# Kernel optimization log

Measured on AMD Instinct MI355X. Metric: run time of the kernel, lower is better.

The kernel has to match this reference:

```python
import jax, jax.numpy as jnp
import numpy as np

IMG_SIZE = 512
NUM_FREQ_MASKS = 4


def _make_masks(n, num):
    # Mirrors DCTTransform._generate_freq_masks: for i in reversed(range(num-1)),
    # an anti-triangular (low-frequency) mask of size n//2**i padded to (n,n),
    # then an all-ones mask appended last.
    masks = []
    for i in reversed(range(num - 1)):
        m = n // (2 ** i)
        tri = np.triu(np.ones((m, m), dtype=np.float32))      # upper triangular
        rot = np.rot90(tri, k=1)                               # -> i+j <= m-1 region
        pad = np.zeros((n, n), dtype=np.float32)
        pad[:m, :m] = rot
        masks.append(pad)
    masks.append(np.ones((n, n), dtype=np.float32))
    return np.stack(masks)  # [num, n, n]


def _dct_matrix(n, dtype=jnp.float32):
    # Orthonormal DCT-II matrix: X = D @ x  ==  scipy.fftpack.dct(x, axis=0, norm='ortho')
    k = jnp.arange(n, dtype=dtype)[:, None]
    m = jnp.arange(n, dtype=dtype)[None, :]
    D = jnp.cos(jnp.pi * (2.0 * m + 1.0) * k / (2.0 * n)) * jnp.sqrt(2.0 / n)
    D = D.at[0].multiply(1.0 / jnp.sqrt(2.0))  # k=0 row scale -> sqrt(1/n)
    return D


def setup_inputs() -> dict:
    key = jax.random.key(0)
    x = jax.random.normal(key, (32, 3, IMG_SIZE, IMG_SIZE), dtype=jnp.float32)
    masks = jnp.asarray(_make_masks(IMG_SIZE, NUM_FREQ_MASKS))
    return {"x": x, "masks": masks}


def reference(x, masks):
    # x: [B, C, H, W] with H == W == img_size; masks: [4, H, W]
    n = x.shape[-1]
    D = _dct_matrix(n, x.dtype)
    # 2D orthonormal DCT-II over last two axes: D @ x @ D^T (separable, order-free)
    dct2 = jnp.einsum('ij,bcjk,lk->bcil', D, x, D)
    outs = []
    for i in range(masks.shape[0]):  # small fixed loop over 4 masks
        masked = dct2 * masks[i]
        # inverse 2D DCT (IDCT-II == DCT-III, orthonormal): D^T @ y @ D
        outs.append(jnp.einsum('ji,bcjk,kl->bcil', D, masked, D))
    LH, HL, HH, LL = outs  # idx 0->LH, 1->HL, 2->HH, 3(ones)->LL per original forward
    return (LL, LH, HL, HH)
```

## Files before the change

kernel.cpp:

```cpp
#include <hip/hip_runtime.h>
#include <hip/hip_bf16.h>
#include <stdint.h>

#define NIMG 96
#define N 512
#define IMG (N*N)
#define OUT_PLANE ((long long)NIMG * IMG)

typedef __attribute__((ext_vector_type(8))) _Float16 f16x8;
typedef __attribute__((ext_vector_type(4))) float f32x4;
typedef unsigned short u16;

__device__ inline u16 f2h(float v) {
    _Float16 h = (_Float16)v;
    return __builtin_bit_cast(u16, h);
}

__device__ inline void gload16(const void* g, void* l) {
    __builtin_amdgcn_global_load_lds(
        (const __attribute__((address_space(1))) void*)g,
        (__attribute__((address_space(3))) void*)l, 16, 0, 0);
}

__global__ void build_D(u16* __restrict__ Drm, u16* __restrict__ Dcm) {
    int idx = blockIdx.x * 256 + threadIdx.x;
    int k = idx >> 9, m = idx & 511;
    int r = ((2 * m + 1) * k) & 2047;
    float c = cospif((float)r * (1.0f / 1024.0f));
    float s = (k == 0) ? 0.04419417382415922f : 0.0625f;
    u16 h = f2h(c * s);
    Drm[k * 512 + m] = h;
    Dcm[m * 512 + k] = h;
}

__global__ __launch_bounds__(256) void conv_x(const float* __restrict__ x,
                                              u16* __restrict__ Xcm,
                                              float* __restrict__ outLL) {
    __shared__ float t[32][33];
    const long long base = (long long)blockIdx.z * IMG;
    const int r0 = blockIdx.y * 32, c0 = blockIdx.x * 32;
    const int tr = threadIdx.x >> 3;
    const int tc = (threadIdx.x & 7) * 4;
    float4 v = *(const float4*)&x[base + (long long)(r0 + tr) * N + c0 + tc];
    *(float4*)&outLL[base + (long long)(r0 + tr) * N + c0 + tc] = v;
    t[tr][tc + 0] = v.x; t[tr][tc + 1] = v.y;
    t[tr][tc + 2] = v.z; t[tr][tc + 3] = v.w;
    __syncthreads();
    ushort4 h;
    h.x = f2h(t[tc + 0][tr]); h.y = f2h(t[tc + 1][tr]);
    h.z = f2h(t[tc + 2][tr]); h.w = f2h(t[tc + 3][tr]);
    *(ushort4*)&Xcm[base + (long long)(c0 + tr) * N + r0 + tc] = h;
}

template<int EPI>
__global__ __launch_bounds__(256) void gemm16(
    const u16* __restrict__ A, long long sA, int lda,
    const u16* __restrict__ B, long long sB, int ldb,
    void* __restrict__ Cv, long long sC, int ldc,
    int K, int trilim, int kcap,
    u16* __restrict__ Y2, u16* __restrict__ Y3)
{
    __shared__ u16 As[2][128 * 32];
    __shared__ u16 Bs[2][128 * 32];

    const int bz = blockIdx.z;
    const int m0 = blockIdx.y * 128;
    const int n0 = blockIdx.x * 128;
    const int tid = threadIdx.x;
    const int wave = tid >> 6;
    const int lane = tid & 63;

    const u16* __restrict__ Ab = A + (long long)bz * sA;
    const u16* __restrict__ Bb = B + (long long)bz * sB;

    const int srow = lane >> 2;
    const int sc8  = (lane & 3) * 8;
    const int war  = wave * 32;

    const int fr  = lane & 15;
    const int kg8 = (lane >> 4) * 8;
    const int wr  = (wave >> 1) * 64;
    const int wc  = (wave & 1) * 64;

    int aoff[4], boff[4];
    #pragma unroll
    for (int i = 0; i < 4; ++i) {
        aoff[i] = (wr + i * 16 + fr) * 32 + kg8;
        boff[i] = (wc + i * 16 + fr) * 32 + kg8;
    }

    f32x4 acc[4][4];
    #pragma unroll
    for (int i = 0; i < 4; ++i)
        #pragma unroll
        for (int j = 0; j < 4; ++j)
            acc[i][j] = (f32x4){0.0f, 0.0f, 0.0f, 0.0f};

    const bool skip = (EPI == 3) && (m0 + n0 > trilim);
    const int Keff = (kcap - m0 < K) ? (kcap - m0) : K;

    if (!skip) {
        auto stage = [&](int buf, int k0) {
            #pragma unroll
            for (int i = 0; i < 2; ++i) {
                int r = war + i * 16;
                gload16(Ab + (long long)(m0 + r + srow) * lda + k0 + sc8, &As[buf][r * 32]);
                gload16(Bb + (long long)(n0 + r + srow) * ldb + k0 + sc8, &Bs[buf][r * 32]);
            }
        };
        auto compute = [&](int buf) {
            f16x8 af[4], bf[4];
            #pragma unroll
            for (int i = 0; i < 4; ++i) af[i] = *(const f16x8*)&As[buf][aoff[i]];
            #pragma unroll
            for (int j = 0; j < 4; ++j) bf[j] = *(const f16x8*)&Bs[buf][boff[j]];
            #pragma unroll
            for (int i = 0; i < 4; ++i)
                #pragma unroll
                for (int j = 0; j < 4; ++j)
                    acc[i][j] = __builtin_amdgcn_mfma_f32_16x16x32_f16(af[i], bf[j], acc[i][j], 0, 0, 0);
        };

        const int nb = Keff >> 5;
        stage(0, 0);
        __syncthreads();
        int cur = 0;
        for (int t = 0; t < nb - 1; ++t) {
            stage(cur ^ 1, (t + 1) * 32);
            compute(cur);
            __syncthreads();
            cur ^= 1;
        }
        compute(cur);
    }

    const int rb = (lane >> 4) * 4;
    if (EPI == 0) {
        float* Cb = (float*)Cv + (long long)bz * sC;
        #pragma unroll
        for (int i = 0; i < 4; ++i)
            #pragma unroll
            for (int j = 0; j < 4; ++j) {
                int r = m0 + wr + i * 16 + rb;
                int c = n0 + wc + j * 16 + fr;
                #pragma unroll
                for (int g = 0; g < 4; ++g)
                    Cb[(long long)(r + g) * ldc + c] = acc[i][j][g];
            }
    } else if (EPI == 1) {
        u16* Cb = (u16*)Cv + (long long)bz * sC;
        #pragma unroll
        for (int i = 0; i < 4; ++i)
            #pragma unroll
            for (int j = 0; j < 4; ++j) {
                int r = m0 + wr + i * 16 + rb;
                int c = n0 + wc + j * 16 + fr;
                #pragma unroll
                for (int g = 0; g < 4; ++g)
                    Cb[(long long)(r + g) * ldc + c] = f2h(acc[i][j][g]);
            }
    } else {
        u16* Cb = (u16*)Cv + (long long)bz * sC;
        u16* Y2b = (EPI == 3) ? Y2 + (long long)bz * (256 * 256) : nullptr;
        u16* Y3b = (EPI == 3) ? Y3 + (long long)bz * (128 * 128) : nullptr;
        #pragma unroll
        for (int i = 0; i < 4; ++i)
            #pragma unroll
            for (int j = 0; j < 4; ++j) {
                int r = m0 + wr + i * 16 + rb;
                int c = n0 + wc + j * 16 + fr;
                float v0 = ((r + 0) + c <= trilim) ? acc[i][j][0] : 0.0f;
                float v1 = ((r + 1) + c <= trilim) ? acc[i][j][1] : 0.0f;
                float v2 = ((r + 2) + c <= trilim) ? acc[i][j][2] : 0.0f;
                float v3 = ((r + 3) + c <= trilim) ? acc[i][j][3] : 0.0f;
                ushort4 h;
                h.x = f2h(v0); h.y = f2h(v1); h.z = f2h(v2); h.w = f2h(v3);
                *(ushort4*)&Cb[(long long)c * ldc + r] = h;
                if (EPI == 3) {
                    if (r < 256 && c < 256) {
                        ushort4 h2;
                        h2.x = ((r + 0) + c <= 255) ? h.x : (u16)0;
                        h2.y = ((r + 1) + c <= 255) ? h.y : (u16)0;
                        h2.z = ((r + 2) + c <= 255) ? h.z : (u16)0;
                        h2.w = ((r + 3) + c <= 255) ? h.w : (u16)0;
                        *(ushort4*)&Y2b[(long long)c * 256 + r] = h2;
                    }
                    if (r < 128 && c < 128) {
                        ushort4 h3;
                        h3.x = ((r + 0) + c <= 127) ? h.x : (u16)0;
                        h3.y = ((r + 1) + c <= 127) ? h.y : (u16)0;
                        h3.z = ((r + 2) + c <= 127) ? h.z : (u16)0;
                        h3.w = ((r + 3) + c <= 127) ? h.w : (u16)0;
                        *(ushort4*)&Y3b[(long long)c * 128 + r] = h3;
                    }
                }
            }
    }
}

extern "C" void kernel_launch(void* const* d_in, const int* in_sizes, int n_in,
                              void* d_out, int out_size, void* d_ws, size_t ws_size,
                              hipStream_t stream) {
    const float* x = (const float*)d_in[0];
    float* out = (float*)d_out;
    float* outLL = out + 0 * OUT_PLANE;
    float* outLH = out + 1 * OUT_PLANE;
    float* outHL = out + 2 * OUT_PLANE;
    float* outHH = out + 3 * OUT_PLANE;

    char* ws = (char*)d_ws;
    u16* Drm = (u16*)(ws);
    u16* Dcm = (u16*)(ws + 524288);
    u16* Xcm = (u16*)(ws + 1048576);
    u16* Ycm = Xcm;
    char* reg = ws + 51380224;
    u16* T1 = (u16*)reg;
    u16* U  = (u16*)reg;
    u16* U2 = (u16*)reg;
    u16* U3 = (u16*)reg;
    u16* Y2 = (u16*)outLH;
    u16* Y3 = (u16*)outLH + (long long)NIMG * 256 * 256;

    const long long S = IMG;
    const int BIG = 1 << 30;

    build_D<<<dim3(IMG / 256), 256, 0, stream>>>(Drm, Dcm);
    conv_x<<<dim3(16, 16, NIMG), 256, 0, stream>>>(x, Xcm, outLL);

    gemm16<1><<<dim3(4, 4, NIMG), 256, 0, stream>>>(
        Drm, 0, 512, Xcm, S, 512, T1, S, 512, 512, 0, BIG, nullptr, nullptr);
    gemm16<3><<<dim3(4, 4, NIMG), 256, 0, stream>>>(
        T1, S, 512, Drm, 0, 512, Ycm, S, 512, 512, 511, BIG, Y2, Y3);
    gemm16<2><<<dim3(4, 4, NIMG), 256, 0, stream>>>(
        Ycm, S, 512, Dcm, 0, 512, U, S, 512, 512, BIG, 512, nullptr, nullptr);
    gemm16<0><<<dim3(4, 4, NIMG), 256, 0, stream>>>(
        U, S, 512, Dcm, 0, 512, outHH, S, 512, 512, 0, BIG, nullptr, nullptr);

    gemm16<2><<<dim3(4, 2, NIMG), 256, 0, stream>>>(
        Y2, 256 * 256, 256, Dcm, 0, 512, U2, 512 * 256, 256, 256, BIG, 256, nullptr, nullptr);
    gemm16<0><<<dim3(4, 4, NIMG), 256, 0, stream>>>(
        U2, 512 * 256, 256, Dcm, 0, 512, outHL, S, 512, 256, 0, BIG, nullptr, nullptr);

    gemm16<2><<<dim3(4, 1, NIMG), 256, 0, stream>>>(
        Y3, 128 * 128, 128, Dcm, 0, 512, U3, 512 * 128, 128, 128, BIG, BIG, nullptr, nullptr);
    gemm16<0><<<dim3(4, 4, NIMG), 256, 0, stream>>>(
        U3, 512 * 128, 128, Dcm, 0, 512, outLH, S, 512, 128, 0, BIG, nullptr, nullptr);
}
```

Measured before the change: 366.4 us.

## Merge inverse-DCT GEMMs for the three masked bands into batched multi-problem launches

New measurement: 355.2 us. 3.1% less time.

```diff
diff --git a/kernel.cpp b/kernel.cpp
--- a/kernel.cpp
+++ b/kernel.cpp
@@ -11,12 +11,12 @@
 typedef __attribute__((ext_vector_type(4))) float f32x4;
 typedef unsigned short u16;
 
-__device__ inline u16 f2h(float v) {
+__device__ __forceinline__ u16 f2h(float v) {
     _Float16 h = (_Float16)v;
     return __builtin_bit_cast(u16, h);
 }
 
-__device__ inline void gload16(const void* g, void* l) {
+__device__ __forceinline__ void gload16(const void* g, void* l) {
     __builtin_amdgcn_global_load_lds(
         (const __attribute__((address_space(1))) void*)g,
         (__attribute__((address_space(3))) void*)l, 16, 0, 0);
@@ -52,89 +52,88 @@
     *(ushort4*)&Xcm[base + (long long)(c0 + tr) * N + r0 + tc] = h;
 }
 
+#define GEMM_DECLS                                                         \
+    const int tid = threadIdx.x;                                           \
+    const int wave = tid >> 6;                                             \
+    const int lane = tid & 63;                                             \
+    const int srow = lane >> 2;                                            \
+    const int sc8  = (lane & 3) * 8;                                       \
+    const int war  = wave * 32;                                            \
+    const int fr   = lane & 15;                                            \
+    const int kg8  = (lane >> 4) * 8;                                      \
+    const int wr   = (wave >> 1) * 64;                                     \
+    const int wc   = (wave & 1) * 64;                                      \
+    const int rb   = (lane >> 4) * 4;                                      \
+    int aoff[4], boff[4];                                                  \
+    _Pragma("unroll")                                                      \
+    for (int i = 0; i < 4; ++i) {                                          \
+        aoff[i] = (wr + i * 16 + fr) * 32 + kg8;                           \
+        boff[i] = (wc + i * 16 + fr) * 32 + kg8;                           \
+    }                                                                      \
+    f32x4 acc[4][4];                                                       \
+    _Pragma("unroll")                                                      \
+    for (int i = 0; i < 4; ++i)                                            \
+        _Pragma("unroll")                                                  \
+        for (int j = 0; j < 4; ++j)                                        \
+            acc[i][j] = (f32x4){0.0f, 0.0f, 0.0f, 0.0f};
+
+#define GEMM_LOOP(Ab, lda, Bb, ldb, Keff)                                  \
+    {                                                                      \
+        auto stage = [&](int buf, int k0) {                                \
+            _Pragma("unroll")                                              \
+            for (int i = 0; i < 2; ++i) {                                  \
+                int r = war + i * 16;                                      \
+                gload16((Ab) + (long long)(m0 + r + srow) * (lda) + k0 + sc8, &As[buf][r * 32]); \
+                gload16((Bb) + (long long)(n0 + r + srow) * (ldb) + k0 + sc8, &Bs[buf][r * 32]); \
+            }                                                              \
+        };                                                                 \
+        auto compute = [&](int buf) {                                      \
+            f16x8 af[4], bf[4];                                            \
+            _Pragma("unroll")                                              \
+            for (int i = 0; i < 4; ++i) af[i] = *(const f16x8*)&As[buf][aoff[i]]; \
+            _Pragma("unroll")                                              \
+            for (int j = 0; j < 4; ++j) bf[j] = *(const f16x8*)&Bs[buf][boff[j]]; \
+            _Pragma("unroll")                                              \
+            for (int i = 0; i < 4; ++i)                                    \
+                _Pragma("unroll")                                          \
+                for (int j = 0; j < 4; ++j)                                \
+                    acc[i][j] = __builtin_amdgcn_mfma_f32_16x16x32_f16(af[i], bf[j], acc[i][j], 0, 0, 0); \
+        };                                                                 \
+        const int nb = (Keff) >> 5;                                        \
+        stage(0, 0);                                                       \
+        __syncthreads();                                                   \
+        int cur = 0;                                                       \
+        for (int t = 0; t < nb - 1; ++t) {                                 \
+            stage(cur ^ 1, (t + 1) * 32);                                  \
+            compute(cur);                                                  \
+            __syncthreads();                                               \
+            cur ^= 1;                                                      \
+        }                                                                  \
+        compute(cur);                                                      \
+    }
+
 template<int EPI>
 __global__ __launch_bounds__(256) void gemm16(
     const u16* __restrict__ A, long long sA, int lda,
     const u16* __restrict__ B, long long sB, int ldb,
     void* __restrict__ Cv, long long sC, int ldc,
-    int K, int trilim, int kcap,
+    int K, int trilim,
     u16* __restrict__ Y2, u16* __restrict__ Y3)
 {
     __shared__ u16 As[2][128 * 32];
     __shared__ u16 Bs[2][128 * 32];
-
     const int bz = blockIdx.z;
     const int m0 = blockIdx.y * 128;
     const int n0 = blockIdx.x * 128;
-    const int tid = threadIdx.x;
-    const int wave = tid >> 6;
-    const int lane = tid & 63;
+
+    if (EPI == 3 && (m0 + n0 > trilim)) return;
 
     const u16* __restrict__ Ab = A + (long long)bz * sA;
     const u16* __restrict__ Bb = B + (long long)bz * sB;
 
-    const int srow = lane >> 2;
-    const int sc8  = (lane & 3) * 8;
-    const int war  = wave * 32;
-
-    const int fr  = lane & 15;
-    const int kg8 = (lane >> 4) * 8;
-    const int wr  = (wave >> 1) * 64;
-    const int wc  = (wave & 1) * 64;
-
-    int aoff[4], boff[4];
-    #pragma unroll
-    for (int i = 0; i < 4; ++i) {
-        aoff[i] = (wr + i * 16 + fr) * 32 + kg8;
-        boff[i] = (wc + i * 16 + fr) * 32 + kg8;
-    }
-
-    f32x4 acc[4][4];
-    #pragma unroll
-    for (int i = 0; i < 4; ++i)
-        #pragma unroll
-        for (int j = 0; j < 4; ++j)
-            acc[i][j] = (f32x4){0.0f, 0.0f, 0.0f, 0.0f};
-
-    const bool skip = (EPI == 3) && (m0 + n0 > trilim);
-    const int Keff = (kcap - m0 < K) ? (kcap - m0) : K;
-
-    if (!skip) {
-        auto stage = [&](int buf, int k0) {
-            #pragma unroll
-            for (int i = 0; i < 2; ++i) {
-                int r = war + i * 16;
-                gload16(Ab + (long long)(m0 + r + srow) * lda + k0 + sc8, &As[buf][r * 32]);
-                gload16(Bb + (long long)(n0 + r + srow) * ldb + k0 + sc8, &Bs[buf][r * 32]);
-            }
-        };
-        auto compute = [&](int buf) {
-            f16x8 af[4], bf[4];
-            #pragma unroll
-            for (int i = 0; i < 4; ++i) af[i] = *(const f16x8*)&As[buf][aoff[i]];
-            #pragma unroll
-            for (int j = 0; j < 4; ++j) bf[j] = *(const f16x8*)&Bs[buf][boff[j]];
-            #pragma unroll
-            for (int i = 0; i < 4; ++i)
-                #pragma unroll
-                for (int j = 0; j < 4; ++j)
-                    acc[i][j] = __builtin_amdgcn_mfma_f32_16x16x32_f16(af[i], bf[j], acc[i][j], 0, 0, 0);
-        };
-
-        const int nb = Keff >> 5;
-        stage(0, 0);
-        __syncthreads();
-        int cur = 0;
-        for (int t = 0; t < nb - 1; ++t) {
-            stage(cur ^ 1, (t + 1) * 32);
-            compute(cur);
-            __syncthreads();
-            cur ^= 1;
-        }
-        compute(cur);
-    }
-
-    const int rb = (lane >> 4) * 4;
+    GEMM_DECLS
+    GEMM_LOOP(Ab, lda, Bb, ldb, K)
+
     if (EPI == 0) {
         float* Cb = (float*)Cv + (long long)bz * sC;
         #pragma unroll
@@ -161,8 +160,9 @@
             }
     } else {
         u16* Cb = (u16*)Cv + (long long)bz * sC;
-        u16* Y2b = (EPI == 3) ? Y2 + (long long)bz * (256 * 256) : nullptr;
-        u16* Y3b = (EPI == 3) ? Y3 + (long long)bz * (128 * 128) : nullptr;
+        u16* Y2b = Y2 + (long long)bz * (256 * 256);
+        u16* Y3b = Y3 + (long long)bz * (128 * 128);
+        const bool doY2 = (m0 + n0 < 256);
         #pragma unroll
         for (int i = 0; i < 4; ++i)
             #pragma unroll
@@ -176,26 +176,116 @@
                 ushort4 h;
                 h.x = f2h(v0); h.y = f2h(v1); h.z = f2h(v2); h.w = f2h(v3);
                 *(ushort4*)&Cb[(long long)c * ldc + r] = h;
-                if (EPI == 3) {
-                    if (r < 256 && c < 256) {
-                        ushort4 h2;
-                        h2.x = ((r + 0) + c <= 255) ? h.x : (u16)0;
-                        h2.y = ((r + 1) + c <= 255) ? h.y : (u16)0;
-                        h2.z = ((r + 2) + c <= 255) ? h.z : (u16)0;
-                        h2.w = ((r + 3) + c <= 255) ? h.w : (u16)0;
-                        *(ushort4*)&Y2b[(long long)c * 256 + r] = h2;
-                    }
-                    if (r < 128 && c < 128) {
-                        ushort4 h3;
-                        h3.x = ((r + 0) + c <= 127) ? h.x : (u16)0;
-                        h3.y = ((r + 1) + c <= 127) ? h.y : (u16)0;
-                        h3.z = ((r + 2) + c <= 127) ? h.z : (u16)0;
-                        h3.w = ((r + 3) + c <= 127) ? h.w : (u16)0;
-                        *(ushort4*)&Y3b[(long long)c * 128 + r] = h3;
-                    }
+                if (doY2 && r < 256 && c < 256) {
+                    ushort4 h2;
+                    h2.x = ((r + 0) + c <= 255) ? h.x : (u16)0;
+                    h2.y = ((r + 1) + c <= 255) ? h.y : (u16)0;
+                    h2.z = ((r + 2) + c <= 255) ? h.z : (u16)0;
+                    h2.w = ((r + 3) + c <= 255) ? h.w : (u16)0;
+                    *(ushort4*)&Y2b[(long long)c * 256 + r] = h2;
+                }
+                if (r < 128 && c < 128) {
+                    ushort4 h3;
+                    h3.x = ((r + 0) + c <= 127) ? h.x : (u16)0;
+                    h3.y = ((r + 1) + c <= 127) ? h.y : (u16)0;
+                    h3.z = ((r + 2) + c <= 127) ? h.z : (u16)0;
+                    h3.w = ((r + 3) + c <= 127) ? h.w : (u16)0;
+                    *(ushort4*)&Y3b[(long long)c * 128 + r] = h3;
                 }
             }
     }
+}
+
+__global__ __launch_bounds__(256) void invA(
+    const u16* __restrict__ Ycm, const u16* __restrict__ Y2,
+    const u16* __restrict__ Y3, const u16* __restrict__ Dcm,
+    u16* __restrict__ U, u16* __restrict__ U2, u16* __restrict__ U3)
+{
+    __shared__ u16 As[2][128 * 32];
+    __shared__ u16 Bs[2][128 * 32];
+    const int bz = blockIdx.z;
+    const int id = blockIdx.x;
+
+    const u16* __restrict__ Ab;
+    u16* __restrict__ Cb;
+    int lda, ldc, Keff, m0, n0;
+    if (id < 16) {
+        m0 = (id >> 2) * 128; n0 = (id & 3) * 128;
+        Ab = Ycm + (long long)bz * IMG;     lda = 512;
+        Cb = U   + (long long)bz * IMG;     ldc = 512;
+        Keff = 512 - m0;
+    } else if (id < 24) {
+        int t = id - 16;
+        m0 = (t >> 2) * 128; n0 = (t & 3) * 128;
+        Ab = Y2 + (long long)bz * 65536;    lda = 256;
+        Cb = U2 + (long long)bz * 131072;   ldc = 256;
+        Keff = 256 - m0;
+    } else {
+        int t = id - 24;
+        m0 = 0;              n0 = (t & 3) * 128;
+        Ab = Y3 + (long long)bz * 16384;    lda = 128;
+        Cb = U3 + (long long)bz * 65536;    ldc = 128;
+        Keff = 128;
+    }
+    const u16* __restrict__ Bb = Dcm;
+    const int ldb = 512;
+
+    GEMM_DECLS
+    GEMM_LOOP(Ab, lda, Bb, ldb, Keff)
+
+    #pragma unroll
+    for (int i = 0; i < 4; ++i)
+        #pragma unroll
+        for (int j = 0; j < 4; ++j) {
+            int r = m0 + wr + i * 16 + rb;
+            int c = n0 + wc + j * 16 + fr;
+            ushort4 h;
+            h.x = f2h(acc[i][j][0]); h.y = f2h(acc[i][j][1]);
+            h.z = f2h(acc[i][j][2]); h.w = f2h(acc[i][j][3]);
+            *(ushort4*)&Cb[(long long)c * ldc + r] = h;
+        }
+}
+
+__global__ __launch_bounds__(256) void invB(
+    const u16* __restrict__ U2, const u16* __restrict__ U3,
+    const u16* __restrict__ Dcm,
+    float* __restrict__ outHL, float* __restrict__ outLH)
+{
+    __shared__ u16 As[2][128 * 32];
+    __shared__ u16 Bs[2][128 * 32];
+    const int bz = blockIdx.z;
+    const int id = blockIdx.x;
+
+    const u16* __restrict__ Ab;
+    float* __restrict__ Cb;
+    int lda, Keff, m0, n0;
+    if (id < 16) {
+        m0 = (id >> 2) * 128; n0 = (id & 3) * 128;
+        Ab = U2 + (long long)bz * 131072;  lda = 256; Keff = 256;
+        Cb = outHL + (long long)bz * IMG;
+    } else {
+        int t = id - 16;
+        m0 = (t >> 2) * 128; n0 = (t & 3) * 128;
+        Ab = U3 + (long long)bz * 65536;   lda = 128; Keff = 128;
+        Cb = outLH + (long long)bz * IMG;
+    }
+    const u16* __restrict__ Bb = Dcm;
+    const int ldb = 512;
+    const int ldc = 512;
+
+    GEMM_DECLS
+    GEMM_LOOP(Ab, lda, Bb, ldb, Keff)
+
+    #pragma unroll
+    for (int i = 0; i < 4; ++i)
+        #pragma unroll
+        for (int j = 0; j < 4; ++j) {
+            int r = m0 + wr + i * 16 + rb;
+            int c = n0 + wc + j * 16 + fr;
+            #pragma unroll
+            for (int g = 0; g < 4; ++g)
+                Cb[(long long)(r + g) * ldc + c] = acc[i][j][g];
+        }
 }
 
 extern "C" void kernel_launch(void* const* d_in, const int* in_sizes, int n_in,
@@ -216,10 +306,11 @@
     char* reg = ws + 51380224;
     u16* T1 = (u16*)reg;
     u16* U  = (u16*)reg;
-    u16* U2 = (u16*)reg;
-    u16* U3 = (u16*)reg;
-    u16* Y2 = (u16*)outLH;
-    u16* Y3 = (u16*)outLH + (long long)NIMG * 256 * 256;
+
+    u16* Y2 = (u16*)outHH;
+    u16* Y3 = Y2 + 6291456;
+    u16* U2 = Y3 + 1572864;
+    u16* U3 = U2 + 12582912;
 
     const long long S = IMG;
     const int BIG = 1 << 30;
@@ -228,21 +319,11 @@
     conv_x<<<dim3(16, 16, NIMG), 256, 0, stream>>>(x, Xcm, outLL);
 
     gemm16<1><<<dim3(4, 4, NIMG), 256, 0, stream>>>(
-        Drm, 0, 512, Xcm, S, 512, T1, S, 512, 512, 0, BIG, nullptr, nullptr);
+        Drm, 0, 512, Xcm, S, 512, T1, S, 512, 512, BIG, nullptr, nullptr);
     gemm16<3><<<dim3(4, 4, NIMG), 256, 0, stream>>>(
-        T1, S, 512, Drm, 0, 512, Ycm, S, 512, 512, 511, BIG, Y2, Y3);
-    gemm16<2><<<dim3(4, 4, NIMG), 256, 0, stream>>>(
-        Ycm, S, 512, Dcm, 0, 512, U, S, 512, 512, BIG, 512, nullptr, nullptr);
+        T1, S, 512, Drm, 0, 512, Ycm, S, 512, 512, 511, Y2, Y3);
+    invA<<<dim3(28, 1, NIMG), 256, 0, stream>>>(Ycm, Y2, Y3, Dcm, U, U2, U3);
+    invB<<<dim3(32, 1, NIMG), 256, 0, stream>>>(U2, U3, Dcm, outHL, outLH);
     gemm16<0><<<dim3(4, 4, NIMG), 256, 0, stream>>>(
-        U, S, 512, Dcm, 0, 512, outHH, S, 512, 512, 0, BIG, nullptr, nullptr);
-
-    gemm16<2><<<dim3(4, 2, NIMG), 256, 0, stream>>>(
-        Y2, 256 * 256, 256, Dcm, 0, 512, U2, 512 * 256, 256, 256, BIG, 256, nullptr, nullptr);
-    gemm16<0><<<dim3(4, 4, NIMG), 256, 0, stream>>>(
-        U2, 512 * 256, 256, Dcm, 0, 512, outHL, S, 512, 256, 0, BIG, nullptr, nullptr);
-
-    gemm16<2><<<dim3(4, 1, NIMG), 256, 0, stream>>>(
-        Y3, 128 * 128, 128, Dcm, 0, 512, U3, 512 * 128, 128, 128, BIG, BIG, nullptr, nullptr);
-    gemm16<0><<<dim3(4, 4, NIMG), 256, 0, stream>>>(
-        U3, 512 * 128, 128, Dcm, 0, 512, outLH, S, 512, 128, 0, BIG, nullptr, nullptr);
-}
+        U, S, 512, Dcm, 0, 512, outHH, S, 512, 512, BIG, nullptr, nullptr);
+}
```
